# Kernel tuning notes

Hardware: AMD Instinct MI355X
Metric: run time of the kernel (lower is better)

The kernel has to match this reference:

```python
import jax, jax.numpy as jnp
import numpy as np

D_MODEL = 768
D_STATE = 16
D_CONV = 4
EXPAND = 2
INNER = EXPAND * D_MODEL  # 1536
BATCH = 2
SEQLEN = 2048


def setup_inputs() -> dict:
    key = jax.random.key(0)
    ks = jax.random.split(key, 8)
    s = 0.02
    return {
        "hidden_states": jax.random.normal(ks[0], (BATCH, SEQLEN, D_MODEL), jnp.float32),
        "in_proj_w": jax.random.normal(ks[1], (2 * INNER, D_MODEL), jnp.float32) * (D_MODEL ** -0.5),
        "out_proj_w": jax.random.normal(ks[2], (D_MODEL, INNER), jnp.float32) * (INNER ** -0.5),
        "dt_proj_w": jax.random.normal(ks[3], (INNER, INNER), jnp.float32) * (INNER ** -0.5),
        "dt_proj_b": jnp.zeros((INNER,), jnp.float32),
        "conv_w": jax.random.normal(ks[4], (INNER, D_CONV), jnp.float32) * s,
        "conv_b": jnp.zeros((INNER,), jnp.float32),
        "A_log": jnp.zeros((INNER, D_STATE), jnp.float32),
        "B_param": jax.random.normal(ks[5], (INNER, D_STATE), jnp.float32) * s,
        "C_param": jax.random.normal(ks[6], (INNER, D_STATE), jnp.float32) * s,
        "D_param": jnp.ones((INNER,), jnp.float32),
        "dt_bias": jnp.zeros((INNER,), jnp.float32),
    }


def reference(hidden_states, in_proj_w, out_proj_w, dt_proj_w, dt_proj_b,
              conv_w, conv_b, A_log, B_param, C_param, D_param, dt_bias):
    # in_proj: (B, L, d_model) -> (B, L, 2*inner); split into projected / gate
    xz = jnp.einsum('bld,od->blo', hidden_states, in_proj_w)
    proj, gate = jnp.split(xz, 2, axis=-1)
    x = jnp.transpose(proj, (0, 2, 1))  # (B, inner, L) channel-first

    # depthwise causal conv (left-pad d_conv-1) + bias + SiLU
    conv = jax.lax.conv_general_dilated(
        x, conv_w[:, None, :], window_strides=(1,),
        padding=[(D_CONV - 1, 0)], feature_group_count=INNER,
        dimension_numbers=('NCH', 'OIH', 'NCH'))
    u = jax.nn.silu(conv + conv_b[None, :, None])  # (B, inner, L)

    # dt projection (1x1 linear on channel-first) + softplus(dt + dt_bias)
    delta = jnp.einsum('oc,bcl->bol', dt_proj_w, u) + dt_proj_b[None, :, None]
    dt = jax.nn.softplus(delta + dt_bias[None, :, None])  # (B, inner, L)

    A = -jnp.exp(A_log)  # (inner, d_state)
    # discretize: dA = exp(dt * A), dBu = dt * u * B   -> (B, inner, L, N)
    dA = jnp.exp(dt[..., None] * A[None, :, None, :])
    dBu = (dt * u)[..., None] * B_param[None, :, None, :]

    dA_t = jnp.moveaxis(dA, 2, 0)    # (L, B, inner, N)
    dBu_t = jnp.moveaxis(dBu, 2, 0)  # (L, B, inner, N)

    def step(h, inp):
        a_t, b_t = inp
        h = a_t * h + b_t                      # (B, inner, N)
        y = jnp.einsum('bdn,dn->bd', h, C_param)
        return h, y

    h0 = jnp.zeros(dA_t.shape[1:], dA.dtype)
    _, ys = jax.lax.scan(step, h0, (dA_t, dBu_t))  # ys: (L, B, inner)
    y = jnp.transpose(ys, (1, 2, 0))               # (B, inner, L)

    z = jnp.transpose(gate, (0, 2, 1))             # (B, inner, L)
    y = (y + D_param[None, :, None] * u) * jax.nn.silu(z)

    # out_proj: (B, inner, L) -> (B, L, d_model)
    return jnp.einsum('bdl,od->blo', y, out_proj_w)
```

## Files before the change

kernel.cpp:

```cpp
#include <hip/hip_runtime.h>
#include <cstdint>
#include <cstddef>

#define D_MODEL 768
#define D_STATE 16
#define D_CONV  4
#define INNER   1536
#define BATCH   2
#define SEQLEN  2048
#define M_TOK   (BATCH * SEQLEN)
#define NCH     (BATCH * INNER)
#define NCHUNK  64
#define CL      (SEQLEN / NCHUNK)

typedef unsigned short u16;
typedef __attribute__((ext_vector_type(4))) unsigned short us4;
typedef __attribute__((ext_vector_type(8))) short bf8;
typedef __attribute__((ext_vector_type(4))) float f32x4;

__device__ __forceinline__ u16 f2bf(float f) {
    uint32_t x = __float_as_uint(f);
    return (u16)((x + 0x7fffu + ((x >> 16) & 1u)) >> 16);
}
__device__ __forceinline__ float bf2f(u16 h) {
    return __uint_as_float(((uint32_t)h) << 16);
}

__global__ __launch_bounds__(256) void cvt_hilo(
    const float* __restrict__ x, u16* __restrict__ hi, u16* __restrict__ lo, int n4)
{
    const int i = blockIdx.x * 256 + threadIdx.x;
    if (i >= n4) return;
    const float4 v = ((const float4*)x)[i];
    us4 h, l;
    h.x = f2bf(v.x); l.x = f2bf(v.x - bf2f(h.x));
    h.y = f2bf(v.y); l.y = f2bf(v.y - bf2f(h.y));
    h.z = f2bf(v.z); l.z = f2bf(v.z - bf2f(h.z));
    h.w = f2bf(v.w); l.w = f2bf(v.w - bf2f(h.w));
    ((us4*)hi)[i] = h;
    ((us4*)lo)[i] = l;
}

template <int MODE, int FRM>
__global__ __launch_bounds__(256) void gemm_mfma(
    const u16* __restrict__ Ah_g, const u16* __restrict__ Al_g,
    const u16* __restrict__ Bh_g, const u16* __restrict__ Bl_g,
    float* __restrict__ C, const float* __restrict__ bias1,
    const float* __restrict__ bias2, int M, int N, int K)
{
    constexpr int BM = FRM * 32;
    constexpr int SBUF = (BM + 128) * 128;
    __shared__ __align__(16) char smem[2 * SBUF];

    const int tid = threadIdx.x;
    const int w = tid >> 6;
    const int lane = tid & 63;

    const int gx = gridDim.x;
    const int nwg = gx * gridDim.y;
    int f = blockIdx.y * gx + blockIdx.x;
    f = (f & 7) * (nwg >> 3) + (f >> 3);
    const int bm = (f / gx) * BM;
    const int bn = (f % gx) * 128;

    const int wm = (w >> 1) * (FRM * 16);
    const int wn = (w & 1) * 64;

    const int g8 = lane & 7;
    const int r8 = lane >> 3;
    const int src = g8 ^ r8;
    const int scol = (src & 3) * 8;
    const bool use_lo = (src & 4) != 0;

    const u16* pA[FRM];
    const u16* pB[4];
#pragma unroll
    for (int c = 0; c < FRM; ++c) {
        const int row = w * (FRM * 8) + c * 8 + r8;
        pA[c] = (use_lo ? Al_g : Ah_g) + (size_t)(bm + row) * K + scol;
    }
#pragma unroll
    for (int c = 0; c < 4; ++c) {
        const int row = w * 32 + c * 8 + r8;
        pB[c] = (use_lo ? Bl_g : Bh_g) + (size_t)(bn + row) * K + scol;
    }

    f32x4 acc[FRM][4] = {};
    const int fr = lane & 15;
    const int gk = lane >> 4;
    const int ghi = gk ^ (fr & 7);

    const int nt = K >> 5;

#define STAGE_ALL(p, kt)                                                            \
    {                                                                               \
        char* sb = smem + (p) * SBUF;                                               \
        _Pragma("unroll")                                                           \
        for (int c = 0; c < FRM; ++c)                                               \
            __builtin_amdgcn_global_load_lds(                                       \
                (const __attribute__((address_space(1))) void*)(pA[c] + (kt)),      \
                (__attribute__((address_space(3))) void*)(sb + (w * FRM + c) * 1024), \
                16, 0, 0);                                                          \
        _Pragma("unroll")                                                           \
        for (int c = 0; c < 4; ++c)                                                 \
            __builtin_amdgcn_global_load_lds(                                       \
                (const __attribute__((address_space(1))) void*)(pB[c] + (kt)),      \
                (__attribute__((address_space(3))) void*)(sb + BM * 128 + (w * 4 + c) * 1024), \
                16, 0, 0);                                                          \
    }

    STAGE_ALL(0, 0)

    int p = 0;
    for (int t = 0; t < nt; ++t) {
        if (t + 1 < nt) {
            STAGE_ALL(p ^ 1, (t + 1) * 32)
            if constexpr (FRM == 4) {
                asm volatile("s_waitcnt vmcnt(8)" ::: "memory");
            } else {
                asm volatile("s_waitcnt vmcnt(6)" ::: "memory");
            }
        } else {
            asm volatile("s_waitcnt vmcnt(0)" ::: "memory");
        }
        __builtin_amdgcn_s_barrier();
        __builtin_amdgcn_sched_barrier(0);

        const char* A0 = smem + p * SBUF;
        const char* B0 = A0 + BM * 128;
        bf8 ah[FRM], al[FRM], bh[4], bl[4];
#pragma unroll
        for (int i = 0; i < FRM; ++i) {
            const int row = wm + i * 16 + fr;
            ah[i] = *(const bf8*)(A0 + row * 128 + ghi * 16);
            al[i] = *(const bf8*)(A0 + row * 128 + (ghi ^ 4) * 16);
        }
#pragma unroll
        for (int j = 0; j < 4; ++j) {
            const int row = wn + j * 16 + fr;
            bh[j] = *(const bf8*)(B0 + row * 128 + ghi * 16);
            bl[j] = *(const bf8*)(B0 + row * 128 + (ghi ^ 4) * 16);
        }
#pragma unroll
        for (int i = 0; i < FRM; ++i)
#pragma unroll
            for (int j = 0; j < 4; ++j) {
                acc[i][j] = __builtin_amdgcn_mfma_f32_16x16x32_bf16(ah[i], bh[j], acc[i][j], 0, 0, 0);
                acc[i][j] = __builtin_amdgcn_mfma_f32_16x16x32_bf16(ah[i], bl[j], acc[i][j], 0, 0, 0);
                acc[i][j] = __builtin_amdgcn_mfma_f32_16x16x32_bf16(al[i], bh[j], acc[i][j], 0, 0, 0);
            }

        __builtin_amdgcn_sched_barrier(0);
        __builtin_amdgcn_s_barrier();
        p ^= 1;
    }
#undef STAGE_ALL

    const int r0 = (lane >> 4) * 4;
#pragma unroll
    for (int i = 0; i < FRM; ++i) {
        const int row0 = bm + wm + i * 16 + r0;
#pragma unroll
        for (int j = 0; j < 4; ++j) {
            const int col = bn + wn + j * 16 + fr;
            float add = 0.f;
            if constexpr (MODE == 1) add = bias1[col] + bias2[col];
#pragma unroll
            for (int r = 0; r < 4; ++r) {
                float v = acc[i][j][r];
                if constexpr (MODE == 1) {
                    const float xx = v + add;
                    v = (xx > 20.f) ? xx : log1pf(expf(xx));
                }
                C[(size_t)(row0 + r) * N + col] = v;
            }
        }
    }
}

__global__ __launch_bounds__(256) void conv_silu_kernel(
    const float* __restrict__ xz, const float* __restrict__ cw,
    const float* __restrict__ cb, u16* __restrict__ uh, u16* __restrict__ ul)
{
    const int idx = blockIdx.x * 256 + threadIdx.x;
    const int c4 = (idx % (INNER / 4)) * 4;
    const int m  = idx / (INNER / 4);
    if (m >= M_TOK) return;
    const int b = m >> 11;
    const int l = m & (SEQLEN - 1);

    float wt[4][4];
#pragma unroll
    for (int i = 0; i < 4; ++i) {
        const float4 wv = *(const float4*)&cw[(c4 + i) * 4];
        wt[i][0] = wv.x; wt[i][1] = wv.y; wt[i][2] = wv.z; wt[i][3] = wv.w;
    }
    const float4 bias = *(const float4*)&cb[c4];
    float a[4] = {bias.x, bias.y, bias.z, bias.w};

#pragma unroll
    for (int j = 0; j < 4; ++j) {
        const int ll = l - 3 + j;
        if (ll >= 0) {
            const float4 x = *(const float4*)&xz[(size_t)(b * SEQLEN + ll) * (2 * INNER) + c4];
            a[0] = fmaf(x.x, wt[0][j], a[0]);
            a[1] = fmaf(x.y, wt[1][j], a[1]);
            a[2] = fmaf(x.z, wt[2][j], a[2]);
            a[3] = fmaf(x.w, wt[3][j], a[3]);
        }
    }
    float o[4];
#pragma unroll
    for (int i = 0; i < 4; ++i) o[i] = a[i] / (1.f + __expf(-a[i]));

    us4 h, lo;
    h.x = f2bf(o[0]); lo.x = f2bf(o[0] - bf2f(h.x));
    h.y = f2bf(o[1]); lo.y = f2bf(o[1] - bf2f(h.y));
    h.z = f2bf(o[2]); lo.z = f2bf(o[2] - bf2f(h.z));
    h.w = f2bf(o[3]); lo.w = f2bf(o[3] - bf2f(h.w));
    const size_t vi = ((size_t)m * INNER + c4) / 4;
    ((us4*)uh)[vi] = h;
    ((us4*)ul)[vi] = lo;
}

__global__ __launch_bounds__(256) void scan_pass1(
    const float* __restrict__ dt, const u16* __restrict__ uh,
    const u16* __restrict__ ul, const float* __restrict__ A_log,
    const float* __restrict__ Bp, float* __restrict__ hend,
    float* __restrict__ Sdt)
{
    const int ch = blockIdx.x * 256 + threadIdx.x;
    const int c = blockIdx.y;
    const int b = (ch >= INNER) ? 1 : 0;
    const int d = ch - b * INNER;

    float A2[D_STATE], Bn[D_STATE];
#pragma unroll
    for (int n = 0; n < D_STATE; n += 4) {
        const float4 av = *(const float4*)&A_log[d * D_STATE + n];
        const float4 bv = *(const float4*)&Bp[d * D_STATE + n];
        A2[n+0] = -expf(av.x) * 1.44269504f; Bn[n+0] = bv.x;
        A2[n+1] = -expf(av.y) * 1.44269504f; Bn[n+1] = bv.y;
        A2[n+2] = -expf(av.z) * 1.44269504f; Bn[n+2] = bv.z;
        A2[n+3] = -expf(av.w) * 1.44269504f; Bn[n+3] = bv.w;
    }

    const size_t base = (size_t)(b * SEQLEN + c * CL) * INNER + d;
    const float* dtp = dt + base;
    const u16* uhp = uh + base;
    const u16* ulp = ul + base;

    float h[D_STATE] = {};
    float S = 0.f;

    float dtv = dtp[0];
    float uv = bf2f(uhp[0]) + bf2f(ulp[0]);

    for (int l = 0; l < CL; ++l) {
        float dtn = 0.f, un = 0.f;
        if (l + 1 < CL) {
            dtn = dtp[(size_t)(l + 1) * INNER];
            un = bf2f(uhp[(size_t)(l + 1) * INNER]) + bf2f(ulp[(size_t)(l + 1) * INNER]);
        }
        const float dtu = dtv * uv;
        S += dtv;
#pragma unroll
        for (int n = 0; n < D_STATE; ++n) {
            const float dA = exp2f(dtv * A2[n]);
            h[n] = fmaf(dA, h[n], dtu * Bn[n]);
        }
        dtv = dtn; uv = un;
    }

#pragma unroll
    for (int n = 0; n < D_STATE; ++n)
        hend[((size_t)c * D_STATE + n) * NCH + ch] = h[n];
    Sdt[(size_t)c * NCH + ch] = S;
}

__global__ __launch_bounds__(256) void scan_combine(
    const float* __restrict__ hend, const float* __restrict__ Sdt,
    const float* __restrict__ A_log, float* __restrict__ h0all)
{
    const int idx = blockIdx.x * 256 + threadIdx.x;
    const int n = idx / NCH;
    const int ch = idx - n * NCH;
    const int b = (ch >= INNER) ? 1 : 0;
    const int d = ch - b * INNER;
    const float A2 = -expf(A_log[d * D_STATE + n]) * 1.44269504f;

    float h0 = 0.f;
    for (int c = 0; c < NCHUNK; ++c) {
        const size_t o = ((size_t)c * D_STATE + n) * NCH + ch;
        h0all[o] = h0;
        const float P = exp2f(A2 * Sdt[(size_t)c * NCH + ch]);
        h0 = fmaf(P, h0, hend[o]);
    }
}

__global__ __launch_bounds__(256) void scan_pass2(
    const float* __restrict__ dt, const u16* __restrict__ uh,
    const u16* __restrict__ ul, const float* __restrict__ xz,
    const float* __restrict__ A_log, const float* __restrict__ Bp,
    const float* __restrict__ Cp, const float* __restrict__ Dp,
    const float* __restrict__ h0all, u16* __restrict__ ygh,
    u16* __restrict__ ygl)
{
    const int ch = blockIdx.x * 256 + threadIdx.x;
    const int c = blockIdx.y;
    const int b = (ch >= INNER) ? 1 : 0;
    const int d = ch - b * INNER;

    float A2[D_STATE], Bn[D_STATE], Cn[D_STATE];
#pragma unroll
    for (int n = 0; n < D_STATE; n += 4) {
        const float4 av = *(const float4*)&A_log[d * D_STATE + n];
        const float4 bv = *(const float4*)&Bp[d * D_STATE + n];
        const float4 cv = *(const float4*)&Cp[d * D_STATE + n];
        A2[n+0] = -expf(av.x) * 1.44269504f; Bn[n+0] = bv.x; Cn[n+0] = cv.x;
        A2[n+1] = -expf(av.y) * 1.44269504f; Bn[n+1] = bv.y; Cn[n+1] = cv.y;
        A2[n+2] = -expf(av.z) * 1.44269504f; Bn[n+2] = bv.z; Cn[n+2] = cv.z;
        A2[n+3] = -expf(av.w) * 1.44269504f; Bn[n+3] = bv.w; Cn[n+3] = cv.w;
    }
    const float Dd = Dp[d];

    float h[D_STATE];
#pragma unroll
    for (int n = 0; n < D_STATE; ++n)
        h[n] = h0all[((size_t)c * D_STATE + n) * NCH + ch];

    const size_t base = (size_t)(b * SEQLEN + c * CL) * INNER + d;
    const float* dtp = dt + base;
    const u16* uhp = uh + base;
    const u16* ulp = ul + base;
    const float* zp = xz + (size_t)(b * SEQLEN + c * CL) * (2 * INNER) + INNER + d;
    u16* yhp = ygh + base;
    u16* ylp = ygl + base;

    float dtv = dtp[0];
    float uv = bf2f(uhp[0]) + bf2f(ulp[0]);
    float zv = zp[0];

    for (int l = 0; l < CL; ++l) {
        float dtn = 0.f, un = 0.f, zn = 0.f;
        if (l + 1 < CL) {
            dtn = dtp[(size_t)(l + 1) * INNER];
            un = bf2f(uhp[(size_t)(l + 1) * INNER]) + bf2f(ulp[(size_t)(l + 1) * INNER]);
            zn = zp[(size_t)(l + 1) * (2 * INNER)];
        }
        const float dtu = dtv * uv;
        float y = 0.f;
#pragma unroll
        for (int n = 0; n < D_STATE; ++n) {
            const float dA = exp2f(dtv * A2[n]);
            h[n] = fmaf(dA, h[n], dtu * Bn[n]);
            y = fmaf(h[n], Cn[n], y);
        }
        const float sig = 1.f / (1.f + __expf(-zv));
        const float val = (y + Dd * uv) * (zv * sig);
        const u16 hv = f2bf(val);
        yhp[(size_t)l * INNER] = hv;
        ylp[(size_t)l * INNER] = f2bf(val - bf2f(hv));
        dtv = dtn; uv = un; zv = zn;
    }
}

extern "C" void kernel_launch(void* const* d_in, const int* in_sizes, int n_in,
                              void* d_out, int out_size, void* d_ws, size_t ws_size,
                              hipStream_t stream)
{
    const float* hs      = (const float*)d_in[0];
    const float* in_w    = (const float*)d_in[1];
    const float* out_w   = (const float*)d_in[2];
    const float* dt_w    = (const float*)d_in[3];
    const float* dt_b    = (const float*)d_in[4];
    const float* conv_w  = (const float*)d_in[5];
    const float* conv_b  = (const float*)d_in[6];
    const float* A_log   = (const float*)d_in[7];
    const float* Bp      = (const float*)d_in[8];
    const float* Cp      = (const float*)d_in[9];
    const float* Dp      = (const float*)d_in[10];
    const float* dt_bias = (const float*)d_in[11];
    float* out = (float*)d_out;

    float* xz    = (float*)d_ws;
    float* dtf   = xz + (size_t)M_TOK * 2 * INNER;
    float* hend  = dtf + (size_t)M_TOK * INNER;
    float* Sdt   = hend + (size_t)NCHUNK * D_STATE * NCH;
    float* h0all = Sdt + (size_t)NCHUNK * NCH;
    u16* uh  = (u16*)(h0all + (size_t)NCHUNK * D_STATE * NCH);
    u16* ul  = uh  + (size_t)M_TOK * INNER;
    u16* hsh = ul  + (size_t)M_TOK * INNER;
    u16* hsl = hsh + (size_t)M_TOK * D_MODEL;
    u16* ygh = hsl + (size_t)M_TOK * D_MODEL;
    u16* ygl = ygh + (size_t)M_TOK * INNER;
    u16* iwh = ygl + (size_t)M_TOK * INNER;
    u16* iwl = iwh + (size_t)2 * INNER * D_MODEL;
    u16* dwh = iwl + (size_t)2 * INNER * D_MODEL;
    u16* dwl = dwh + (size_t)INNER * INNER;
    u16* owh = dwl + (size_t)INNER * INNER;
    u16* owl = owh + (size_t)D_MODEL * INNER;

    const dim3 blk(256);

    cvt_hilo<<<dim3(M_TOK * D_MODEL / 4 / 256), blk, 0, stream>>>(hs, hsh, hsl, M_TOK * D_MODEL / 4);
    cvt_hilo<<<dim3(2 * INNER * D_MODEL / 4 / 256), blk, 0, stream>>>(in_w, iwh, iwl, 2 * INNER * D_MODEL / 4);
    cvt_hilo<<<dim3(INNER * INNER / 4 / 256), blk, 0, stream>>>(dt_w, dwh, dwl, INNER * INNER / 4);
    cvt_hilo<<<dim3(D_MODEL * INNER / 4 / 256), blk, 0, stream>>>(out_w, owh, owl, D_MODEL * INNER / 4);

    gemm_mfma<0, 4><<<dim3(2 * INNER / 128, M_TOK / 128), blk, 0, stream>>>(
        hsh, hsl, iwh, iwl, xz, nullptr, nullptr, M_TOK, 2 * INNER, D_MODEL);

    conv_silu_kernel<<<dim3((M_TOK * (INNER / 4)) / 256), blk, 0, stream>>>(
        xz, conv_w, conv_b, uh, ul);

    gemm_mfma<1, 4><<<dim3(INNER / 128, M_TOK / 128), blk, 0, stream>>>(
        uh, ul, dwh, dwl, dtf, dt_b, dt_bias, M_TOK, INNER, INNER);

    scan_pass1<<<dim3(NCH / 256, NCHUNK), blk, 0, stream>>>(
        dtf, uh, ul, A_log, Bp, hend, Sdt);
    scan_combine<<<dim3((D_STATE * NCH) / 256), blk, 0, stream>>>(
        hend, Sdt, A_log, h0all);
    scan_pass2<<<dim3(NCH / 256, NCHUNK), blk, 0, stream>>>(
        dtf, uh, ul, xz, A_log, Bp, Cp, Dp, h0all, ygh, ygl);

    gemm_mfma<0, 2><<<dim3(D_MODEL / 128, M_TOK / 64), blk, 0, stream>>>(
        ygh, ygl, owh, owl, out, nullptr, nullptr, M_TOK, D_MODEL, INNER);
}
```

Measured before the change: 340.2 us.

## Merge four conversion launches and single-buffer the GEMM LDS staging

Fuses the four fp32-to-bf16 hi/lo conversion launches into one kernel that picks its source by global index, removing three launch overheads. It also replaces the double-buffered global_load_lds pipeline in the GEMM with a single buffer and a full vmcnt(0) wait plus two syncthreads per K step. Halving LDS may allow more resident workgroups, but the next tile's loads no longer overlap the MFMA work on the current one.

```diff
diff --git a/kernel.cpp b/kernel.cpp
--- a/kernel.cpp
+++ b/kernel.cpp
@@ -26,19 +26,36 @@
     return __uint_as_float(((uint32_t)h) << 16);
 }
 
-__global__ __launch_bounds__(256) void cvt_hilo(
-    const float* __restrict__ x, u16* __restrict__ hi, u16* __restrict__ lo, int n4)
-{
-    const int i = blockIdx.x * 256 + threadIdx.x;
-    if (i >= n4) return;
-    const float4 v = ((const float4*)x)[i];
+__global__ __launch_bounds__(256) void cvt_hilo4(
+    const float* __restrict__ s0, u16* __restrict__ h0, u16* __restrict__ l0, int n0,
+    const float* __restrict__ s1, u16* __restrict__ h1, u16* __restrict__ l1, int n1,
+    const float* __restrict__ s2, u16* __restrict__ h2, u16* __restrict__ l2, int n2,
+    const float* __restrict__ s3, u16* __restrict__ h3, u16* __restrict__ l3, int n3)
+{
+    int j = blockIdx.x * 256 + threadIdx.x;
+    const float* s; u16* hh; u16* ll;
+    if (j < n0) { s = s0; hh = h0; ll = l0; }
+    else {
+        j -= n0;
+        if (j < n1) { s = s1; hh = h1; ll = l1; }
+        else {
+            j -= n1;
+            if (j < n2) { s = s2; hh = h2; ll = l2; }
+            else {
+                j -= n2;
+                if (j >= n3) return;
+                s = s3; hh = h3; ll = l3;
+            }
+        }
+    }
+    const float4 v = ((const float4*)s)[j];
     us4 h, l;
     h.x = f2bf(v.x); l.x = f2bf(v.x - bf2f(h.x));
     h.y = f2bf(v.y); l.y = f2bf(v.y - bf2f(h.y));
     h.z = f2bf(v.z); l.z = f2bf(v.z - bf2f(h.z));
     h.w = f2bf(v.w); l.w = f2bf(v.w - bf2f(h.w));
-    ((us4*)hi)[i] = h;
-    ((us4*)lo)[i] = l;
+    ((us4*)hh)[j] = h;
+    ((us4*)ll)[j] = l;
 }
 
 template <int MODE, int FRM>
@@ -50,7 +67,7 @@
 {
     constexpr int BM = FRM * 32;
     constexpr int SBUF = (BM + 128) * 128;
-    __shared__ __align__(16) char smem[2 * SBUF];
+    __shared__ __align__(16) char smem[SBUF];
 
     const int tid = threadIdx.x;
     const int w = tid >> 6;
@@ -90,44 +107,25 @@
     const int gk = lane >> 4;
     const int ghi = gk ^ (fr & 7);
 
-    const int nt = K >> 5;
-
-#define STAGE_ALL(p, kt)                                                            \
-    {                                                                               \
-        char* sb = smem + (p) * SBUF;                                               \
-        _Pragma("unroll")                                                           \
-        for (int c = 0; c < FRM; ++c)                                               \
-            __builtin_amdgcn_global_load_lds(                                       \
-                (const __attribute__((address_space(1))) void*)(pA[c] + (kt)),      \
-                (__attribute__((address_space(3))) void*)(sb + (w * FRM + c) * 1024), \
-                16, 0, 0);                                                          \
-        _Pragma("unroll")                                                           \
-        for (int c = 0; c < 4; ++c)                                                 \
-            __builtin_amdgcn_global_load_lds(                                       \
-                (const __attribute__((address_space(1))) void*)(pB[c] + (kt)),      \
-                (__attribute__((address_space(3))) void*)(sb + BM * 128 + (w * 4 + c) * 1024), \
-                16, 0, 0);                                                          \
-    }
-
-    STAGE_ALL(0, 0)
-
-    int p = 0;
-    for (int t = 0; t < nt; ++t) {
-        if (t + 1 < nt) {
-            STAGE_ALL(p ^ 1, (t + 1) * 32)
-            if constexpr (FRM == 4) {
-                asm volatile("s_waitcnt vmcnt(8)" ::: "memory");
-            } else {
-                asm volatile("s_waitcnt vmcnt(6)" ::: "memory");
-            }
-        } else {
-            asm volatile("s_waitcnt vmcnt(0)" ::: "memory");
-        }
-        __builtin_amdgcn_s_barrier();
-        __builtin_amdgcn_sched_barrier(0);
-
-        const char* A0 = smem + p * SBUF;
-        const char* B0 = A0 + BM * 128;
+    for (int k0 = 0; k0 < K; k0 += 32) {
+        __syncthreads();
+#pragma unroll
+        for (int c = 0; c < FRM; ++c)
+            __builtin_amdgcn_global_load_lds(
+                (const __attribute__((address_space(1))) void*)(pA[c] + k0),
+                (__attribute__((address_space(3))) void*)(smem + (w * FRM + c) * 1024),
+                16, 0, 0);
+#pragma unroll
+        for (int c = 0; c < 4; ++c)
+            __builtin_amdgcn_global_load_lds(
+                (const __attribute__((address_space(1))) void*)(pB[c] + k0),
+                (__attribute__((address_space(3))) void*)(smem + BM * 128 + (w * 4 + c) * 1024),
+                16, 0, 0);
+        asm volatile("s_waitcnt vmcnt(0)" ::: "memory");
+        __syncthreads();
+
+        const char* A0 = smem;
+        const char* B0 = smem + BM * 128;
         bf8 ah[FRM], al[FRM], bh[4], bl[4];
 #pragma unroll
         for (int i = 0; i < FRM; ++i) {
@@ -149,12 +147,7 @@
                 acc[i][j] = __builtin_amdgcn_mfma_f32_16x16x32_bf16(ah[i], bl[j], acc[i][j], 0, 0, 0);
                 acc[i][j] = __builtin_amdgcn_mfma_f32_16x16x32_bf16(al[i], bh[j], acc[i][j], 0, 0, 0);
             }
-
-        __builtin_amdgcn_sched_barrier(0);
-        __builtin_amdgcn_s_barrier();
-        p ^= 1;
-    }
-#undef STAGE_ALL
+    }
 
     const int r0 = (lane >> 4) * 4;
 #pragma unroll
@@ -403,10 +396,16 @@
 
     const dim3 blk(256);
 
-    cvt_hilo<<<dim3(M_TOK * D_MODEL / 4 / 256), blk, 0, stream>>>(hs, hsh, hsl, M_TOK * D_MODEL / 4);
-    cvt_hilo<<<dim3(2 * INNER * D_MODEL / 4 / 256), blk, 0, stream>>>(in_w, iwh, iwl, 2 * INNER * D_MODEL / 4);
-    cvt_hilo<<<dim3(INNER * INNER / 4 / 256), blk, 0, stream>>>(dt_w, dwh, dwl, INNER * INNER / 4);
-    cvt_hilo<<<dim3(D_MODEL * INNER / 4 / 256), blk, 0, stream>>>(out_w, owh, owl, D_MODEL * INNER / 4);
+    {
+        const int n0 = M_TOK * D_MODEL / 4;
+        const int n1 = 2 * INNER * D_MODEL / 4;
+        const int n2 = INNER * INNER / 4;
+        const int n3 = D_MODEL * INNER / 4;
+        const int ntot = n0 + n1 + n2 + n3;
+        cvt_hilo4<<<dim3((ntot + 255) / 256), blk, 0, stream>>>(
+            hs, hsh, hsl, n0, in_w, iwh, iwl, n1,
+            dt_w, dwh, dwl, n2, out_w, owh, owl, n3);
+    }
 
     gemm_mfma<0, 4><<<dim3(2 * INNER / 128, M_TOK / 128), blk, 0, stream>>>(
         hsh, hsl, iwh, iwl, xz, nullptr, nullptr, M_TOK, 2 * INNER, D_MODEL);
```

New measurement: 341.3 us. About the same (+0.3%).
